# Optimization experiments

Measured on AMD Instinct MI355X. Metric: run time of the kernel, lower is better.

## Reference

```python
import jax, jax.numpy as jnp
import numpy as np
from jax import lax

B, D_MODEL, H, W = 8, 384, 64, 64
D_INNER, D_STATE, D_CONV, DT_RANK = 768, 16, 4, 24
C3, MLP_H = 3 * D_MODEL, 4 * D_MODEL
EPS = 1e-5


def setup_inputs():
    key = jax.random.key(0)
    ks = jax.random.split(key, 16)
    r = lambda i, shape, s=0.02: jax.random.normal(ks[i], shape, jnp.float32) * s
    return {
        'x': jax.random.normal(ks[0], (B, D_MODEL, H, W), jnp.float32),
        'ln1_g': jnp.ones((D_MODEL,), jnp.float32), 'ln1_b': jnp.zeros((D_MODEL,), jnp.float32),
        'in_w': r(1, (2 * D_INNER, D_MODEL)),
        'conv_w': r(2, (D_INNER, 1, D_CONV), 0.2), 'conv_b': jnp.zeros((D_INNER,), jnp.float32),
        'xproj_w': r(3, (DT_RANK + 2 * D_STATE, D_INNER)),
        'dtproj_w': r(4, (D_INNER, DT_RANK), 0.1),
        'dtproj_b': jnp.full((D_INNER,), jnp.log(jnp.expm1(0.01)).item(), jnp.float32),
        'A_log': jnp.log(jnp.broadcast_to(jnp.arange(1, D_STATE + 1, dtype=jnp.float32), (D_INNER, D_STATE))),
        'Dskip': jnp.ones((D_INNER,), jnp.float32),
        'out_w': r(5, (D_MODEL, D_INNER)),
        'dw_w': r(6, (C3, 1, 3, 3), 0.1),
        'bn_g': jnp.ones((C3,), jnp.float32), 'bn_b': jnp.zeros((C3,), jnp.float32),
        'bn_mean': jnp.zeros((C3,), jnp.float32), 'bn_var': jnp.ones((C3,), jnp.float32),
        'pw_w': r(7, (C3, C3)),
        'fus_w': r(8, (D_MODEL, D_MODEL)), 'fus_b': jnp.zeros((D_MODEL,), jnp.float32),
        'ln2_g': jnp.ones((D_MODEL,), jnp.float32), 'ln2_b': jnp.zeros((D_MODEL,), jnp.float32),
        'mlp_w1': r(9, (MLP_H, D_MODEL)), 'mlp_b1': jnp.zeros((MLP_H,), jnp.float32),
        'mlp_w2': r(10, (D_MODEL, MLP_H)), 'mlp_b2': jnp.zeros((D_MODEL,), jnp.float32),
    }


def _ln(x, g, b):
    m = x.mean(-1, keepdims=True)
    v = ((x - m) ** 2).mean(-1, keepdims=True)
    return (x - m) / jnp.sqrt(v + EPS) * g + b


def _dwt(x):
    x01 = x[:, :, 0::2, :] / 2
    x02 = x[:, :, 1::2, :] / 2
    x1, x3 = x01[:, :, :, 0::2], x01[:, :, :, 1::2]
    x2, x4 = x02[:, :, :, 0::2], x02[:, :, :, 1::2]
    ll = x1 + x2 + x3 + x4
    hl = -x1 - x2 + x3 + x4
    lh = -x1 + x2 - x3 + x4
    hh = x1 - x2 - x3 + x4
    return ll, jnp.concatenate([hl, lh, hh], axis=1)


def _idwt(ll, high):
    b, c, h, w = ll.shape
    hl, lh, hh = jnp.split(high, 3, axis=1)
    h_ll, h_hl, h_lh, h_hh = ll / 2, hl / 2, lh / 2, hh / 2
    y1 = h_ll - h_hl - h_lh + h_hh  # (even row, even col)
    y2 = h_ll - h_hl + h_lh - h_hh  # (odd row, even col)
    y3 = h_ll + h_hl - h_lh - h_hh  # (even row, odd col)
    y4 = h_ll + h_hl + h_lh + h_hh  # (odd row, odd col)
    row_e = jnp.stack([y1, y3], axis=-1).reshape(b, c, h, 2 * w)
    row_o = jnp.stack([y2, y4], axis=-1).reshape(b, c, h, 2 * w)
    return jnp.stack([row_e, row_o], axis=-2).reshape(b, c, 2 * h, 2 * w)


def _mamba(x, in_w, conv_w, conv_b, xproj_w, dtproj_w, dtproj_b, A_log, Dskip, out_w):
    # x: [B, L, d_model]
    bb = x.shape[0]
    xz = x @ in_w.T  # [B,L,2*d_inner]
    xi, z = jnp.split(xz, 2, axis=-1)
    xc = jnp.swapaxes(xi, 1, 2)  # [B,d_inner,L]
    xc = lax.conv_general_dilated(xc, conv_w, (1,), [(D_CONV - 1, 0)],
                                  feature_group_count=D_INNER,
                                  dimension_numbers=('NCH', 'OIH', 'NCH')) + conv_b[None, :, None]
    u = jax.nn.silu(jnp.swapaxes(xc, 1, 2))  # [B,L,d_inner]
    dbl = u @ xproj_w.T
    dtr = dbl[..., :DT_RANK]
    Bm = dbl[..., DT_RANK:DT_RANK + D_STATE]
    Cm = dbl[..., DT_RANK + D_STATE:]
    dt = jax.nn.softplus(dtr @ dtproj_w.T + dtproj_b)  # [B,L,d_inner]
    A = -jnp.exp(A_log)  # [d_inner,d_state]

    def step(h, t):
        dt_t, B_t, C_t, u_t = t
        dA = jnp.exp(dt_t[:, :, None] * A)
        h = dA * h + (dt_t * u_t)[:, :, None] * B_t[:, None, :]
        return h, jnp.sum(h * C_t[:, None, :], axis=-1)

    h0 = jnp.zeros((bb, D_INNER, D_STATE), x.dtype)
    xs = (jnp.swapaxes(dt, 0, 1), jnp.swapaxes(Bm, 0, 1), jnp.swapaxes(Cm, 0, 1), jnp.swapaxes(u, 0, 1))
    _, ys = lax.scan(step, h0, xs)
    y = jnp.swapaxes(ys, 0, 1) + u * Dskip
    y = y * jax.nn.silu(z)
    return y @ out_w.T


def reference(x, ln1_g, ln1_b, in_w, conv_w, conv_b, xproj_w, dtproj_w, dtproj_b,
              A_log, Dskip, out_w, dw_w, bn_g, bn_b, bn_mean, bn_var, pw_w,
              fus_w, fus_b, ln2_g, ln2_b, mlp_w1, mlp_b1, mlp_w2, mlp_b2):
    shortcut = x
    x_ll, x_high = _dwt(x)
    b, c, hh, ww = x_ll.shape
    # LL branch: LN -> Mamba -> residual
    x_ll_in = _ln(jnp.transpose(x_ll, (0, 2, 3, 1)), ln1_g, ln1_b)
    y = _mamba(x_ll_in.reshape(b, hh * ww, c), in_w, conv_w, conv_b, xproj_w,
               dtproj_w, dtproj_b, A_log, Dskip, out_w)
    x_ll_out = x_ll + jnp.transpose(y.reshape(b, hh, ww, c), (0, 3, 1, 2))
    # High-freq branch: depthwise3x3 -> BN(eval) -> SiLU -> 1x1 -> residual
    hd = lax.conv_general_dilated(x_high, dw_w, (1, 1), [(1, 1), (1, 1)],
                                  feature_group_count=C3,
                                  dimension_numbers=('NCHW', 'OIHW', 'NCHW'))
    hd = (hd - bn_mean[None, :, None, None]) / jnp.sqrt(bn_var + EPS)[None, :, None, None] \
         * bn_g[None, :, None, None] + bn_b[None, :, None, None]
    hd = jax.nn.silu(hd)
    x_high_out = x_high + jnp.einsum('bchw,oc->bohw', hd, pw_w)
    # Reconstruct + fusion 1x1 conv + residual
    recon = _idwt(x_ll_out, x_high_out)
    recon = jnp.einsum('bchw,oc->bohw', recon, fus_w) + fus_b[None, :, None, None]
    x2 = shortcut + recon
    # LN + MLP + residual
    xn = _ln(jnp.transpose(x2, (0, 2, 3, 1)), ln2_g, ln2_b)
    m = jax.nn.gelu(xn @ mlp_w1.T + mlp_b1, approximate=False) @ mlp_w2.T + mlp_b2
    return x2 + jnp.transpose(m, (0, 3, 1, 2))
```

## Files before the change

### kernel.cpp

```cpp
#include <hip/hip_runtime.h>
#include <hip/hip_bf16.h>
#include <math.h>

typedef __hip_bfloat16 bf16;
typedef __attribute__((ext_vector_type(8))) short bf16x8;
typedef __attribute__((ext_vector_type(4))) float f32x4;
typedef unsigned short u16;

#define LN_EPS 1e-5f

__device__ inline u16 f2b(float v) {
    __hip_bfloat16 h = __float2bfloat16(v);
    return *reinterpret_cast<u16*>(&h);
}

__device__ inline float b2f_lo(unsigned int w) { return __uint_as_float(w << 16); }
__device__ inline float b2f_hi(unsigned int w) { return __uint_as_float(w & 0xFFFF0000u); }

__device__ inline void gload_lds16(const void* g, void* l) {
    __builtin_amdgcn_global_load_lds(
        (const __attribute__((address_space(1))) void*)(uintptr_t)g,
        (__attribute__((address_space(3))) void*)(uintptr_t)(unsigned int)(uintptr_t)l,
        16, 0, 0);
}

__global__ __launch_bounds__(256) void sentinel_kernel(float* __restrict__ out, int n) {
    int i = blockIdx.x * 256 + threadIdx.x;
    if (i < n) out[i] = 123.0f;
}

__global__ __launch_bounds__(256) void reduce12_kernel(const float* __restrict__ P,
                                                       float* __restrict__ out, int n4) {
    int i = blockIdx.x * 256 + threadIdx.x;
    if (i >= n4) return;
    const float4* p4 = (const float4*)P;
    float4 s = p4[i];
#pragma unroll
    for (int z = 1; z < 12; z++) {
        float4 v = p4[(size_t)z * n4 + i];
        s.x += v.x; s.y += v.y; s.z += v.z; s.w += v.w;
    }
    ((float4*)out)[i] = s;
}

__global__ void detect_kernel(const unsigned int* __restrict__ g, int* __restrict__ flag) {
    *flag = (*g == 0x3F803F80u) ? 1 : 0;
}

struct Jobs {
    const void* src[25];
    int prefix[26];
};
__global__ __launch_bounds__(256) void convert_kernel(Jobs J, u16* __restrict__ dst16,
                                                      float* __restrict__ dst32,
                                                      const int* __restrict__ flag) {
    int i = blockIdx.x * 256 + threadIdx.x;
    int total = J.prefix[25];
    if (i >= total) return;
    int f = *flag;
    int lo = 0;
    while (J.prefix[lo + 1] <= i) lo++;
    int off = i - J.prefix[lo];
    float v = f ? (float)((const bf16*)J.src[lo])[off] : ((const float*)J.src[lo])[off];
    if (lo < 6) dst16[i] = f2b(v);
    else        dst32[i - J.prefix[6]] = v;
}

__global__ __launch_bounds__(256) void dwt_kernel(const void* __restrict__ xv,
                                                  float* __restrict__ xll,
                                                  float* __restrict__ xhigh,
                                                  const int* __restrict__ flag) {
    __shared__ float tile[32][133];
    int blk = blockIdx.x;
    int cc = blk % 12;
    int t2 = blk / 12;
    int i  = t2 % 32;
    int b  = t2 / 32;
    int t  = threadIdx.x;
    int c_l = t >> 3;
    int sub = t & 7;
    size_t rowbase = ((size_t)(b * 384 + cc * 32 + c_l)) * 4096 + (size_t)i * 128;
    if (*flag) {
        const u16* xp = (const u16*)xv + rowbase;
#pragma unroll
        for (int k = 0; k < 2; k++) {
            int e0 = (sub + k * 8) * 8;
            uint4 v = *(const uint4*)(xp + e0);
            tile[c_l][e0 + 0] = b2f_lo(v.x); tile[c_l][e0 + 1] = b2f_hi(v.x);
            tile[c_l][e0 + 2] = b2f_lo(v.y); tile[c_l][e0 + 3] = b2f_hi(v.y);
            tile[c_l][e0 + 4] = b2f_lo(v.z); tile[c_l][e0 + 5] = b2f_hi(v.z);
            tile[c_l][e0 + 6] = b2f_lo(v.w); tile[c_l][e0 + 7] = b2f_hi(v.w);
        }
    } else {
        const float* xp = (const float*)xv + rowbase;
#pragma unroll
        for (int k = 0; k < 4; k++) {
            int f0 = (sub + k * 8) * 4;
            float4 v = *(const float4*)(xp + f0);
            tile[c_l][f0 + 0] = v.x; tile[c_l][f0 + 1] = v.y;
            tile[c_l][f0 + 2] = v.z; tile[c_l][f0 + 3] = v.w;
        }
    }
    __syncthreads();
    int c_out = t & 31;
    int jg = t >> 5;
    int cg = cc * 32 + c_out;
#pragma unroll
    for (int jj = 0; jj < 4; jj++) {
        int j = jg * 4 + jj;
        float A = tile[c_out][2 * j];
        float B = tile[c_out][2 * j + 1];
        float C = tile[c_out][64 + 2 * j];
        float D = tile[c_out][64 + 2 * j + 1];
        float ll = 0.5f * (A + B + C + D);
        float hl = 0.5f * (B + D - A - C);
        float lh = 0.5f * (C + D - A - B);
        float hh = 0.5f * (A + D - B - C);
        int pm = b * 1024 + i * 32 + j;
        xll[(size_t)pm * 384 + cg] = ll;
        size_t hb = (size_t)pm * 1152;
        xhigh[hb + cg] = hl;
        xhigh[hb + 384 + cg] = lh;
        xhigh[hb + 768 + cg] = hh;
    }
}

template <bool OBF>
__global__ __launch_bounds__(128) void ln_kernel(const float* __restrict__ in,
                                                 void* __restrict__ outv,
                                                 const float* __restrict__ g,
                                                 const float* __restrict__ b) {
    const int C = 384;
    int row = blockIdx.x;
    int t = threadIdx.x;
    const float* rp = in + (size_t)row * C;
    float v0 = rp[t], v1 = rp[t + 128], v2 = rp[t + 256];
    __shared__ float red[128];
    red[t] = v0 + v1 + v2;
    __syncthreads();
    for (int off = 64; off > 0; off >>= 1) {
        if (t < off) red[t] += red[t + off];
        __syncthreads();
    }
    float mean = red[0] * (1.f / 384.f);
    __syncthreads();
    float d0 = v0 - mean, d1 = v1 - mean, d2 = v2 - mean;
    red[t] = d0 * d0 + d1 * d1 + d2 * d2;
    __syncthreads();
    for (int off = 64; off > 0; off >>= 1) {
        if (t < off) red[t] += red[t + off];
        __syncthreads();
    }
    float inv = rsqrtf(red[0] * (1.f / 384.f) + LN_EPS);
    float o0 = d0 * inv * g[t]       + b[t];
    float o1 = d1 * inv * g[t + 128] + b[t + 128];
    float o2 = d2 * inv * g[t + 256] + b[t + 256];
    if constexpr (OBF) {
        u16* op = (u16*)outv + (size_t)row * C;
        op[t] = f2b(o0); op[t + 128] = f2b(o1); op[t + 256] = f2b(o2);
    } else {
        float* op = (float*)outv + (size_t)row * C;
        op[t] = o0; op[t + 128] = o1; op[t + 256] = o2;
    }
}

#define EP_NONE 0
#define EP_SOFTPLUS_BIAS 1
#define EP_ADD 2
#define EP_FUS 3
#define EP_GELU_BIAS 4
#define EP_FINAL 5

template <int EPIL, bool CBF>
__global__ __launch_bounds__(256) void gemm_mfma(const u16* __restrict__ A, int lda,
                                                 const u16* __restrict__ W,
                                                 void* __restrict__ Cp, int ldc,
                                                 int M, int N, int K,
                                                 const float* __restrict__ addsrc,
                                                 const float* __restrict__ bias,
                                                 const void* __restrict__ xres,
                                                 void* __restrict__ obf,
                                                 int m_off,
                                                 const int* __restrict__ flag) {
    __shared__ u16 Als[128][32];
    __shared__ u16 Bls[128][32];
    const int t = threadIdx.x;
    const int wave = t >> 6, lane = t & 63;
    const int quad = lane >> 4, r16 = lane & 15;
    const int wm = (wave >> 1) * 64, wn = (wave & 1) * 64;
    const int mb = blockIdx.y * 128, nb = blockIdx.x * 128;
    f32x4 acc[4][4] = {};

    const int srow = wave * 32 + (lane >> 2);
    const int scol = (lane & 3) * 8;
    const u16* Ag0 = A + (size_t)(mb + srow) * lda + scol;
    const u16* Ag1 = A + (size_t)(mb + srow + 16) * lda + scol;
    const u16* Wg0 = W + (size_t)(nb + srow) * (size_t)K + scol;
    const u16* Wg1 = W + (size_t)(nb + srow + 16) * (size_t)K + scol;
    u16* Al0 = &Als[wave * 32][0];
    u16* Al1 = &Als[wave * 32 + 16][0];
    u16* Bl0 = &Bls[wave * 32][0];
    u16* Bl1 = &Bls[wave * 32 + 16][0];

    for (int k0 = 0; k0 < K; k0 += 32) {
        gload_lds16(Ag0 + k0, Al0);
        gload_lds16(Ag1 + k0, Al1);
        gload_lds16(Wg0 + k0, Bl0);
        gload_lds16(Wg1 + k0, Bl1);
        __syncthreads();
        bf16x8 af[4], bfv[4];
#pragma unroll
        for (int i = 0; i < 4; i++) af[i] = *(const bf16x8*)&Als[wm + i * 16 + r16][quad * 8];
#pragma unroll
        for (int j = 0; j < 4; j++) bfv[j] = *(const bf16x8*)&Bls[wn + j * 16 + r16][quad * 8];
#pragma unroll
        for (int i = 0; i < 4; i++)
#pragma unroll
            for (int j = 0; j < 4; j++)
                acc[i][j] = __builtin_amdgcn_mfma_f32_16x16x32_bf16(af[i], bfv[j], acc[i][j], 0, 0, 0);
        __syncthreads();
    }

    int f = 0;
    if constexpr (EPIL == EP_FUS || EPIL == EP_FINAL) f = *flag;
#pragma unroll
    for (int i = 0; i < 4; i++) {
#pragma unroll
        for (int j = 0; j < 4; j++) {
#pragma unroll
            for (int rg = 0; rg < 4; rg++) {
                int m = mb + wm + i * 16 + quad * 4 + rg;
                int n = nb + wn + j * 16 + r16;
                float v = acc[i][j][rg];
                if constexpr (EPIL == EP_NONE) {
                    if constexpr (CBF) ((u16*)Cp)[(size_t)m * ldc + n] = f2b(v);
                    else               ((float*)Cp)[(size_t)m * ldc + n] = v;
                } else if constexpr (EPIL == EP_ADD) {
                    ((float*)Cp)[(size_t)m * ldc + n] = addsrc[(size_t)m * ldc + n] + v;
                } else if constexpr (EPIL == EP_FUS) {
                    v += bias[n];
                    int bb = m >> 12, pix = m & 4095;
                    size_t xi = ((size_t)(bb * 384 + n) << 12) + pix;
                    v += f ? (float)((const bf16*)xres)[xi] : ((const float*)xres)[xi];
                    ((float*)Cp)[(size_t)m * ldc + n] = v;
                } else if constexpr (EPIL == EP_GELU_BIAS) {
                    v += bias[n];
                    v = 0.5f * v * (1.f + erff(v * 0.70710678118654752f));
                    if constexpr (CBF) ((u16*)Cp)[(size_t)m * ldc + n] = f2b(v);
                    else               ((float*)Cp)[(size_t)m * ldc + n] = v;
                } else if constexpr (EPIL == EP_FINAL) {
                    v += bias[n];
                    int gm = m_off + m;
                    v += addsrc[(size_t)gm * 384 + n];
                    int bb = gm >> 12, pix = gm & 4095;
                    size_t oi = ((size_t)(bb * 384 + n) << 12) + pix;
                    if (f) ((bf16*)obf)[oi] = __float2bfloat16(v);
                    else   ((float*)obf)[oi] = v;
                }
            }
        }
    }
}

template <int EPIL, bool SPLITK>
__global__ __launch_bounds__(256) void gemm_nt(const float* __restrict__ A, int lda,
                                               const float* __restrict__ W,
                                               float* __restrict__ C, int ldc,
                                               int M, int N, int K,
                                               const float* __restrict__ bias,
                                               int kc) {
    __shared__ __align__(16) float As[16][68];
    __shared__ __align__(16) float Bs[16][68];
    int t = threadIdx.x;
    int mb = blockIdx.y * 64;
    int nb = blockIdx.x * 64;
    int kb = SPLITK ? blockIdx.z * kc : 0;
    int ke = SPLITK ? kb + kc : K;
    int tm = t & 15, tn = t >> 4;
    float* Cout = C;
    if constexpr (SPLITK) Cout = C + (size_t)blockIdx.z * (size_t)M * ldc;
    float acc[4][4] = {};
    for (int k0 = kb; k0 < ke; k0 += 16) {
#pragma unroll
        for (int i = 0; i < 4; i++) {
            int idx = t + i * 256;
            int r = idx >> 4, c = idx & 15;
            float v = 0.f;
            if (k0 + c < K) v = A[(size_t)(mb + r) * lda + k0 + c];
            As[c][r] = v;
        }
#pragma unroll
        for (int i = 0; i < 4; i++) {
            int idx = t + i * 256;
            int r = idx >> 4, c = idx & 15;
            float v = 0.f;
            if ((nb + r) < N && (k0 + c) < K) v = W[(size_t)(nb + r) * K + k0 + c];
            Bs[c][r] = v;
        }
        __syncthreads();
#pragma unroll
        for (int kk = 0; kk < 16; kk++) {
            float4 av = *(const float4*)&As[kk][tm * 4];
            float4 bv = *(const float4*)&Bs[kk][tn * 4];
            float a4[4] = {av.x, av.y, av.z, av.w};
            float b4[4] = {bv.x, bv.y, bv.z, bv.w};
#pragma unroll
            for (int i = 0; i < 4; i++)
#pragma unroll
                for (int j = 0; j < 4; j++) acc[i][j] += a4[i] * b4[j];
        }
        __syncthreads();
    }
#pragma unroll
    for (int i = 0; i < 4; i++) {
        int m = mb + tm * 4 + i;
        if (m >= M) continue;
#pragma unroll
        for (int j = 0; j < 4; j++) {
            int n = nb + tn * 4 + j;
            if (n >= N) continue;
            float v = acc[i][j];
            if constexpr (SPLITK) {
                Cout[(size_t)m * ldc + n] = v;
            } else if constexpr (EPIL == EP_NONE) {
                C[(size_t)m * ldc + n] = v;
            } else if constexpr (EPIL == EP_SOFTPLUS_BIAS) {
                v += bias[n];
                v = (v > 20.f) ? v : log1pf(expf(v));
                C[(size_t)m * ldc + n] = v;
            }
        }
    }
}

__global__ __launch_bounds__(256) void conv1d_silu_kernel(const float* __restrict__ xz,
                                                          const float* __restrict__ cw,
                                                          const float* __restrict__ cb,
                                                          float* __restrict__ u) {
    int tid = blockIdx.x * 256 + threadIdx.x;
    int dq = tid % 192;
    int t2 = tid / 192;
    int l = t2 % 1024;
    int b = t2 / 1024;
    int d = dq * 4;
    float4 q0 = *(const float4*)&cw[d * 4];
    float4 q1 = *(const float4*)&cw[d * 4 + 4];
    float4 q2 = *(const float4*)&cw[d * 4 + 8];
    float4 q3 = *(const float4*)&cw[d * 4 + 12];
    float4 acc = *(const float4*)&cb[d];
    int rowbase = b * 1024;
#pragma unroll
    for (int k = 0; k < 4; k++) {
        int ls = l - 3 + k;
        if (ls < 0) continue;
        float4 xv = *(const float4*)&xz[(size_t)(rowbase + ls) * 1536 + d];
        acc.x += ((const float*)&q0)[k] * xv.x;
        acc.y += ((const float*)&q1)[k] * xv.y;
        acc.z += ((const float*)&q2)[k] * xv.z;
        acc.w += ((const float*)&q3)[k] * xv.w;
    }
    float4 o;
    o.x = acc.x / (1.f + __expf(-acc.x));
    o.y = acc.y / (1.f + __expf(-acc.y));
    o.z = acc.z / (1.f + __expf(-acc.z));
    o.w = acc.w / (1.f + __expf(-acc.w));
    *(float4*)&u[(size_t)(rowbase + l) * 768 + d] = o;
}

__device__ inline void scan_load_ac(const float* __restrict__ A_log, int d,
                                    float (&Ac)[16], bool& structured) {
#pragma unroll
    for (int s = 0; s < 16; s++) Ac[s] = -__expf(A_log[d * 16 + s]);
    structured = true;
#pragma unroll
    for (int s = 0; s < 16; s++)
        structured = structured && (fabsf(Ac[s] - (s + 1) * Ac[0]) <= 1e-5f * fabsf(Ac[s]));
}

__global__ __launch_bounds__(256) void scan_p1(const float* __restrict__ dt,
                                               const float* __restrict__ u,
                                               const float* __restrict__ dbl,
                                               const float* __restrict__ A_log,
                                               float* __restrict__ st) {
    int idx = blockIdx.x * 256 + threadIdx.x;
    int g = idx % 6144;
    int c = idx / 6144;
    int d = g % 768, b = g / 768;
    float Ac[16]; bool structured;
    scan_load_ac(A_log, d, Ac, structured);
    float h[16];
#pragma unroll
    for (int s = 0; s < 16; s++) h[s] = 0.f;
    float S = 0.f;
    size_t m0 = (size_t)b * 1024 + c * 128;
    if (structured) {
        for (int j = 0; j < 128; j++) {
            size_t m = m0 + j;
            float dtv = dt[m * 768 + d];
            float uv  = u[m * 768 + d];
            const float4* bp = (const float4*)(dbl + m * 56 + 24);
            float4 B0 = bp[0], B1 = bp[1], B2 = bp[2], B3 = bp[3];
            float Bv[16] = {B0.x,B0.y,B0.z,B0.w, B1.x,B1.y,B1.z,B1.w,
                            B2.x,B2.y,B2.z,B2.w, B3.x,B3.y,B3.z,B3.w};
            float du = dtv * uv;
            S += dtv;
            float q = __expf(dtv * Ac[0]);
            float a = q;
            h[0] = a * h[0] + du * Bv[0];
#pragma unroll
            for (int s = 1; s < 16; s++) { a *= q; h[s] = a * h[s] + du * Bv[s]; }
        }
    } else {
        for (int j = 0; j < 128; j++) {
            size_t m = m0 + j;
            float dtv = dt[m * 768 + d];
            float uv  = u[m * 768 + d];
            const float4* bp = (const float4*)(dbl + m * 56 + 24);
            float4 B0 = bp[0], B1 = bp[1], B2 = bp[2], B3 = bp[3];
            float Bv[16] = {B0.x,B0.y,B0.z,B0.w, B1.x,B1.y,B1.z,B1.w,
                            B2.x,B2.y,B2.z,B2.w, B3.x,B3.y,B3.z,B3.w};
            float du = dtv * uv;
            S += dtv;
#pragma unroll
            for (int s = 0; s < 16; s++) h[s] = __expf(dtv * Ac[s]) * h[s] + du * Bv[s];
        }
    }
    float* stp = st + (size_t)(c * 6144 + g) * 32;
#pragma unroll
    for (int s = 0; s < 16; s++) stp[s] = __expf(Ac[s] * S);
#pragma unroll
    for (int s = 0; s < 16; s++) stp[16 + s] = h[s];
}

__global__ __launch_bounds__(256) void scan_p2(float* __restrict__ st) {
    int tid = blockIdx.x * 256 + threadIdx.x;
    int s = tid & 15;
    int g = tid >> 4;
    float H = 0.f;
#pragma unroll
    for (int c = 0; c < 8; c++) {
        size_t i = (size_t)(c * 6144 + g) * 32;
        float P  = st[i + s];
        float hE = st[i + 16 + s];
        st[i + s] = H;
        H = hE + P * H;
    }
}

__global__ __launch_bounds__(256) void scan_p3(const float* __restrict__ dt,
                                               const float* __restrict__ u,
                                               const float* __restrict__ dbl,
                                               const float* __restrict__ z,
                                               const float* __restrict__ A_log,
                                               const float* __restrict__ Dskip,
                                               const float* __restrict__ st,
                                               u16* __restrict__ ybuf) {
    int idx = blockIdx.x * 256 + threadIdx.x;
    int g = idx % 6144;
    int c = idx / 6144;
    int d = g % 768, b = g / 768;
    float Ac[16]; bool structured;
    scan_load_ac(A_log, d, Ac, structured);
    float Dsk = Dskip[d];
    float h[16];
    const float* stp = st + (size_t)(c * 6144 + g) * 32;
#pragma unroll
    for (int s = 0; s < 16; s++) h[s] = stp[s];
    size_t m0 = (size_t)b * 1024 + c * 128;
    if (structured) {
        for (int j = 0; j < 128; j++) {
            size_t m = m0 + j;
            float dtv = dt[m * 768 + d];
            float uv  = u[m * 768 + d];
            float zv  = z[m * 1536 + 768 + d];
            const float4* bp = (const float4*)(dbl + m * 56 + 24);
            float4 B0 = bp[0], B1 = bp[1], B2 = bp[2], B3 = bp[3];
            float4 C0 = bp[4], C1 = bp[5], C2 = bp[6], C3 = bp[7];
            float Bv[16] = {B0.x,B0.y,B0.z,B0.w, B1.x,B1.y,B1.z,B1.w,
                            B2.x,B2.y,B2.z,B2.w, B3.x,B3.y,B3.z,B3.w};
            float Cv[16] = {C0.x,C0.y,C0.z,C0.w, C1.x,C1.y,C1.z,C1.w,
                            C2.x,C2.y,C2.z,C2.w, C3.x,C3.y,C3.z,C3.w};
            float du = dtv * uv;
            float q = __expf(dtv * Ac[0]);
            float a = q;
            h[0] = a * h[0] + du * Bv[0];
            float y = h[0] * Cv[0];
#pragma unroll
            for (int s = 1; s < 16; s++) {
                a *= q;
                h[s] = a * h[s] + du * Bv[s];
                y += h[s] * Cv[s];
            }
            float sig = 1.f / (1.f + __expf(-zv));
            ybuf[m * 3072 + d] = f2b((y + uv * Dsk) * (zv * sig));
        }
    } else {
        for (int j = 0; j < 128; j++) {
            size_t m = m0 + j;
            float dtv = dt[m * 768 + d];
            float uv  = u[m * 768 + d];
            float zv  = z[m * 1536 + 768 + d];
            const float4* bp = (const float4*)(dbl + m * 56 + 24);
            float4 B0 = bp[0], B1 = bp[1], B2 = bp[2], B3 = bp[3];
            float4 C0 = bp[4], C1 = bp[5], C2 = bp[6], C3 = bp[7];
            float Bv[16] = {B0.x,B0.y,B0.z,B0.w, B1.x,B1.y,B1.z,B1.w,
                            B2.x,B2.y,B2.z,B2.w, B3.x,B3.y,B3.z,B3.w};
            float Cv[16] = {C0.x,C0.y,C0.z,C0.w, C1.x,C1.y,C1.z,C1.w,
                            C2.x,C2.y,C2.z,C2.w, C3.x,C3.y,C3.z,C3.w};
            float du = dtv * uv;
            float y = 0.f;
#pragma unroll
            for (int s = 0; s < 16; s++) {
                h[s] = __expf(dtv * Ac[s]) * h[s] + du * Bv[s];
                y += h[s] * Cv[s];
            }
            float sig = 1.f / (1.f + __expf(-zv));
            ybuf[m * 3072 + d] = f2b((y + uv * Dsk) * (zv * sig));
        }
    }
}

__global__ __launch_bounds__(256) void dwconv_bn_silu_kernel(const float* __restrict__ xh,
                                                             const float* __restrict__ w,
                                                             const float* __restrict__ g,
                                                             const float* __restrict__ bb,
                                                             const float* __restrict__ mean,
                                                             const float* __restrict__ var,
                                                             u16* __restrict__ hd) {
    int tid = blockIdx.x * 256 + threadIdx.x;
    int cq = tid % 288;
    int t2 = tid / 288;
    int xc = t2 & 3;
    int t3 = t2 >> 2;
    int y = t3 % 32;
    int b = t3 / 32;
    int c = cq * 4;
    float wk[9][4];
#pragma unroll
    for (int i = 0; i < 4; i++) {
        float4 wa = *(const float4*)&w[(c + i) * 9];
        float4 wbv = *(const float4*)&w[(c + i) * 9 + 4];
        float wcv = w[(c + i) * 9 + 8];
        wk[0][i] = wa.x; wk[1][i] = wa.y; wk[2][i] = wa.z; wk[3][i] = wa.w;
        wk[4][i] = wbv.x; wk[5][i] = wbv.y; wk[6][i] = wbv.z; wk[7][i] = wbv.w;
        wk[8][i] = wcv;
    }
    float4 mn = *(const float4*)&mean[c];
    float4 vr = *(const float4*)&var[c];
    float4 gg = *(const float4*)&g[c];
    float4 bv = *(const float4*)&bb[c];
    float scl[4], sft[4];
    scl[0] = rsqrtf(vr.x + LN_EPS) * gg.x; sft[0] = bv.x - mn.x * scl[0];
    scl[1] = rsqrtf(vr.y + LN_EPS) * gg.y; sft[1] = bv.y - mn.y * scl[1];
    scl[2] = rsqrtf(vr.z + LN_EPS) * gg.z; sft[2] = bv.z - mn.z * scl[2];
    scl[3] = rsqrtf(vr.w + LN_EPS) * gg.w; sft[3] = bv.w - mn.w * scl[3];

    int x0 = xc * 8;
    size_t pixbase = (size_t)b * 1024 + y * 32;
    float win[3][3][4];
    auto ldcol = [&](int xx, float (&col)[3][4]) {
#pragma unroll
        for (int r = 0; r < 3; r++) {
            int yy = y + r - 1;
            if (xx < 0 || xx > 31 || yy < 0 || yy > 31) {
                col[r][0] = col[r][1] = col[r][2] = col[r][3] = 0.f;
            } else {
                float4 v = *(const float4*)&xh[((size_t)b * 1024 + yy * 32 + xx) * 1152 + c];
                col[r][0] = v.x; col[r][1] = v.y; col[r][2] = v.z; col[r][3] = v.w;
            }
        }
    };
    ldcol(x0 - 1, win[0]);
    ldcol(x0, win[1]);
#pragma unroll
    for (int xi = 0; xi < 8; xi++) {
        int x = x0 + xi;
        ldcol(x + 1, win[2]);
        ushort4 o;
        u16* op = (u16*)&o;
#pragma unroll
        for (int i = 0; i < 4; i++) {
            float acc = 0.f;
#pragma unroll
            for (int ky = 0; ky < 3; ky++)
#pragma unroll
                for (int kx = 0; kx < 3; kx++)
                    acc += wk[ky * 3 + kx][i] * win[kx][ky][i];
            float vv = acc * scl[i] + sft[i];
            op[i] = f2b(vv / (1.f + __expf(-vv)));
        }
        *(ushort4*)&hd[(pixbase + x) * 1152 + c] = o;
#pragma unroll
        for (int r = 0; r < 3; r++)
#pragma unroll
            for (int i = 0; i < 4; i++) {
                win[0][r][i] = win[1][r][i];
                win[1][r][i] = win[2][r][i];
            }
    }
}

__global__ __launch_bounds__(256) void idwt_kernel(const float* __restrict__ xll,
                                                   const float* __restrict__ xh,
                                                   u16* __restrict__ recon) {
    int idx = blockIdx.x * 256 + threadIdx.x;
    int c = idx % 384;
    int t = idx / 384;
    int p = t % 1024;
    int b = t / 1024;
    int i = p >> 5, j = p & 31;
    float ll = xll[(size_t)(b * 1024 + p) * 384 + c];
    int hb = (b * 1024 + p) * 1152;
    float hl = xh[hb + c];
    float lh = xh[hb + 384 + c];
    float hh = xh[hb + 768 + c];
    float y1 = 0.5f * (ll - hl - lh + hh);
    float y3 = 0.5f * (ll + hl - lh - hh);
    float y2 = 0.5f * (ll - hl + lh - hh);
    float y4 = 0.5f * (ll + hl + lh + hh);
    int r0 = b * 4096 + (2 * i) * 64 + 2 * j;
    recon[(size_t)r0 * 384 + c] = f2b(y1);
    recon[(size_t)(r0 + 1) * 384 + c] = f2b(y3);
    recon[(size_t)(r0 + 64) * 384 + c] = f2b(y2);
    recon[(size_t)(r0 + 65) * 384 + c] = f2b(y4);
}

extern "C" void kernel_launch(void* const* d_in, const int* in_sizes, int n_in,
                              void* d_out, int out_size, void* d_ws, size_t ws_size,
                              hipStream_t stream) {
    const void* x = d_in[0];
    void* out = d_out;

    float* ws = (float*)d_ws;
    float* x_ll    = ws;
    float* x_high  = ws + 3145728;
    u16*   mlp_hid = (u16*)ws;
    float* xz      = ws + 12582912;
    u16*   ybuf    = (u16*)xz;
    u16*   hd      = (u16*)xz;
    u16*   recon   = (u16*)(ws + 17301504);
    u16*   xn      = recon;
    float* u       = ws + 25165824;
    float* dt      = ws + 31457280;
    u16*   x_ll_in = (u16*)dt;
    float* xpart   = dt;
    float* x2      = ws + 25165824;
    float* dbl     = ws + 37748736;
    float* scanst  = ws + 38207488;

    u16* wb16 = (u16*)(ws + 39780352);
    u16* b_in_w   = wb16;
    u16* b_out_w  = wb16 + 589824;
    u16* b_pw_w   = wb16 + 884736;
    u16* b_fus_w  = wb16 + 2211840;
    u16* b_mlp_w1 = wb16 + 2359296;
    u16* b_mlp_w2 = wb16 + 2949120;
    float* f32base = ws + 39780352 + 1769472;
    float* c_conv_w   = f32base;
    float* c_conv_b   = f32base + 3072;
    float* c_xproj_w  = f32base + 3840;
    float* c_dtproj_w = f32base + 46848;
    float* c_dtproj_b = f32base + 65280;
    float* c_A_log    = f32base + 66048;
    float* c_Dskip    = f32base + 78336;
    float* c_dw_w     = f32base + 79104;
    float* c_bn_g     = f32base + 89472;
    float* c_bn_b     = f32base + 90624;
    float* c_bn_mean  = f32base + 91776;
    float* c_bn_var   = f32base + 92928;
    float* c_ln1_g    = f32base + 94080;
    float* c_ln1_b    = f32base + 94464;
    float* c_ln2_g    = f32base + 94848;
    float* c_ln2_b    = f32base + 95232;
    float* c_fus_b    = f32base + 95616;
    float* c_mlp_b1   = f32base + 96000;
    float* c_mlp_b2   = f32base + 97536;
    int* flag = (int*)(f32base + 97920);

    if (ws_size < (size_t)(39780352 + 1769472 + 97920 + 2) * 4) {
        sentinel_kernel<<<(out_size + 255) / 256, 256, 0, stream>>>((float*)out, out_size);
        return;
    }

    detect_kernel<<<1, 1, 0, stream>>>((const unsigned int*)d_in[1], flag);
    Jobs J;
    const int src_idx[25] = {3, 11, 17, 18, 22, 24,
                             4, 5, 6, 7, 8, 9, 10, 12, 13, 14, 15, 16,
                             1, 2, 20, 21, 19, 23, 25};
    const int joff[26] = {0, 589824, 884736, 2211840, 2359296, 2949120, 3538944,
                          3538944 + 3072, 3538944 + 3840, 3538944 + 46848, 3538944 + 65280,
                          3538944 + 66048, 3538944 + 78336, 3538944 + 79104, 3538944 + 89472,
                          3538944 + 90624, 3538944 + 91776, 3538944 + 92928, 3538944 + 94080,
                          3538944 + 94464, 3538944 + 94848, 3538944 + 95232, 3538944 + 95616,
                          3538944 + 96000, 3538944 + 97536, 3538944 + 97920};
    for (int i = 0; i < 25; i++) J.src[i] = d_in[src_idx[i]];
    for (int i = 0; i < 26; i++) J.prefix[i] = joff[i];
    convert_kernel<<<(3636864 + 255) / 256, 256, 0, stream>>>(J, wb16, f32base, flag);

    dwt_kernel<<<3072, 256, 0, stream>>>(x, x_ll, x_high, flag);
    ln_kernel<true><<<8192, 128, 0, stream>>>(x_ll, x_ll_in, c_ln1_g, c_ln1_b);
    gemm_mfma<EP_NONE, false><<<dim3(12, 64), 256, 0, stream>>>(x_ll_in, 384, b_in_w, xz, 1536,
                                                                8192, 1536, 384, nullptr, nullptr, nullptr, nullptr, 0, flag);
    conv1d_silu_kernel<<<6144, 256, 0, stream>>>(xz, c_conv_w, c_conv_b, u);
    gemm_nt<EP_NONE, true><<<dim3(1, 128, 12), 256, 0, stream>>>(u, 768, c_xproj_w, xpart, 56,
                                                                 8192, 56, 768, nullptr, 64);
    reduce12_kernel<<<(114688 + 255) / 256, 256, 0, stream>>>(xpart, dbl, 114688);
    gemm_nt<EP_SOFTPLUS_BIAS, false><<<dim3(12, 128), 256, 0, stream>>>(dbl, 56, c_dtproj_w, dt, 768,
                                                                        8192, 768, 24, c_dtproj_b, 0);
    scan_p1<<<192, 256, 0, stream>>>(dt, u, dbl, c_A_log, scanst);
    scan_p2<<<384, 256, 0, stream>>>(scanst);
    scan_p3<<<192, 256, 0, stream>>>(dt, u, dbl, xz, c_A_log, c_Dskip, scanst, ybuf);
    gemm_mfma<EP_ADD, false><<<dim3(3, 64), 256, 0, stream>>>(ybuf, 3072, b_out_w, x_ll, 384,
                                                              8192, 384, 768, x_ll, nullptr, nullptr, nullptr, 0, flag);
    dwconv_bn_silu_kernel<<<1152, 256, 0, stream>>>(x_high, c_dw_w, c_bn_g, c_bn_b, c_bn_mean, c_bn_var, hd);
    gemm_mfma<EP_ADD, false><<<dim3(9, 64), 256, 0, stream>>>(hd, 1152, b_pw_w, x_high, 1152,
                                                              8192, 1152, 1152, x_high, nullptr, nullptr, nullptr, 0, flag);
    idwt_kernel<<<12288, 256, 0, stream>>>(x_ll, x_high, recon);
    gemm_mfma<EP_FUS, false><<<dim3(3, 256), 256, 0, stream>>>(recon, 384, b_fus_w, x2, 384,
                                                               32768, 384, 384, nullptr, c_fus_b, x, nullptr, 0, flag);
    ln_kernel<true><<<32768, 128, 0, stream>>>(x2, xn, c_ln2_g, c_ln2_b);
    for (int ck = 0; ck < 2; ck++) {
        const u16* xn_c = xn + (size_t)ck * 16384 * 384;
        gemm_mfma<EP_GELU_BIAS, true><<<dim3(12, 128), 256, 0, stream>>>(xn_c, 384, b_mlp_w1, mlp_hid, 1536,
                                                                         16384, 1536, 384, nullptr, c_mlp_b1, nullptr, nullptr, 0, flag);
        gemm_mfma<EP_FINAL, false><<<dim3(3, 128), 256, 0, stream>>>(mlp_hid, 1536, b_mlp_w2, nullptr, 0,
                                                                     16384, 384, 1536, x2, c_mlp_b2, nullptr, out, ck * 16384, flag);
    }
}
```

Before: 810.2 us.

## Split selective scan into 16 chunks and store chunk states in xz scratch

The chunked Mamba scan now uses 16 chunks of 64 steps instead of 8 chunks of 128. This doubles the block count of the first and third scan passes from 192 to 384, so more compute units stay busy and each thread runs a shorter serial chain. The per-chunk state, which no longer fits the old scratch area, is written into the already-consumed x half of the xz buffer. The z half is left intact. The sequential loops also get unroll 2, and the cross-chunk combine pass now walks 16 chunks instead of 8.

```diff
diff --git a/kernel.cpp b/kernel.cpp
--- a/kernel.cpp
+++ b/kernel.cpp
@@ -22,6 +22,13 @@
         (const __attribute__((address_space(1))) void*)(uintptr_t)g,
         (__attribute__((address_space(3))) void*)(uintptr_t)(unsigned int)(uintptr_t)l,
         16, 0, 0);
+}
+
+__device__ inline float* st_ptr(float* base, int e) {
+    return base + (size_t)(e / 12) * 1536 + 384 + (e % 12) * 32;
+}
+__device__ inline const float* st_ptr(const float* base, int e) {
+    return base + (size_t)(e / 12) * 1536 + 384 + (e % 12) * 32;
 }
 
 __global__ __launch_bounds__(256) void sentinel_kernel(float* __restrict__ out, int n) {
@@ -381,7 +388,7 @@
                                                const float* __restrict__ u,
                                                const float* __restrict__ dbl,
                                                const float* __restrict__ A_log,
-                                               float* __restrict__ st) {
+                                               float* __restrict__ stbase) {
     int idx = blockIdx.x * 256 + threadIdx.x;
     int g = idx % 6144;
     int c = idx / 6144;
@@ -392,9 +399,10 @@
 #pragma unroll
     for (int s = 0; s < 16; s++) h[s] = 0.f;
     float S = 0.f;
-    size_t m0 = (size_t)b * 1024 + c * 128;
+    size_t m0 = (size_t)b * 1024 + c * 64;
     if (structured) {
-        for (int j = 0; j < 128; j++) {
+#pragma unroll 2
+        for (int j = 0; j < 64; j++) {
             size_t m = m0 + j;
             float dtv = dt[m * 768 + d];
             float uv  = u[m * 768 + d];
@@ -411,7 +419,8 @@
             for (int s = 1; s < 16; s++) { a *= q; h[s] = a * h[s] + du * Bv[s]; }
         }
     } else {
-        for (int j = 0; j < 128; j++) {
+#pragma unroll 2
+        for (int j = 0; j < 64; j++) {
             size_t m = m0 + j;
             float dtv = dt[m * 768 + d];
             float uv  = u[m * 768 + d];
@@ -425,24 +434,24 @@
             for (int s = 0; s < 16; s++) h[s] = __expf(dtv * Ac[s]) * h[s] + du * Bv[s];
         }
     }
-    float* stp = st + (size_t)(c * 6144 + g) * 32;
+    float* stp = st_ptr(stbase, c * 6144 + g);
 #pragma unroll
     for (int s = 0; s < 16; s++) stp[s] = __expf(Ac[s] * S);
 #pragma unroll
     for (int s = 0; s < 16; s++) stp[16 + s] = h[s];
 }
 
-__global__ __launch_bounds__(256) void scan_p2(float* __restrict__ st) {
+__global__ __launch_bounds__(256) void scan_p2(float* __restrict__ stbase) {
     int tid = blockIdx.x * 256 + threadIdx.x;
     int s = tid & 15;
     int g = tid >> 4;
     float H = 0.f;
 #pragma unroll
-    for (int c = 0; c < 8; c++) {
-        size_t i = (size_t)(c * 6144 + g) * 32;
-        float P  = st[i + s];
-        float hE = st[i + 16 + s];
-        st[i + s] = H;
+    for (int c = 0; c < 16; c++) {
+        float* p = st_ptr(stbase, c * 6144 + g);
+        float P  = p[s];
+        float hE = p[16 + s];
+        p[s] = H;
         H = hE + P * H;
     }
 }
@@ -453,7 +462,7 @@
                                                const float* __restrict__ z,
                                                const float* __restrict__ A_log,
                                                const float* __restrict__ Dskip,
-                                               const float* __restrict__ st,
+                                               const float* __restrict__ stbase,
                                                u16* __restrict__ ybuf) {
     int idx = blockIdx.x * 256 + threadIdx.x;
     int g = idx % 6144;
@@ -463,12 +472,13 @@
     scan_load_ac(A_log, d, Ac, structured);
     float Dsk = Dskip[d];
     float h[16];
-    const float* stp = st + (size_t)(c * 6144 + g) * 32;
+    const float* stp = st_ptr(stbase, c * 6144 + g);
 #pragma unroll
     for (int s = 0; s < 16; s++) h[s] = stp[s];
-    size_t m0 = (size_t)b * 1024 + c * 128;
+    size_t m0 = (size_t)b * 1024 + c * 64;
     if (structured) {
-        for (int j = 0; j < 128; j++) {
+#pragma unroll 2
+        for (int j = 0; j < 64; j++) {
             size_t m = m0 + j;
             float dtv = dt[m * 768 + d];
             float uv  = u[m * 768 + d];
@@ -495,7 +505,8 @@
             ybuf[m * 3072 + d] = f2b((y + uv * Dsk) * (zv * sig));
         }
     } else {
-        for (int j = 0; j < 128; j++) {
+#pragma unroll 2
+        for (int j = 0; j < 64; j++) {
             size_t m = m0 + j;
             float dtv = dt[m * 768 + d];
             float uv  = u[m * 768 + d];
@@ -646,7 +657,6 @@
     float* xpart   = dt;
     float* x2      = ws + 25165824;
     float* dbl     = ws + 37748736;
-    float* scanst  = ws + 38207488;
 
     u16* wb16 = (u16*)(ws + 39780352);
     u16* b_in_w   = wb16;
@@ -707,9 +717,9 @@
     reduce12_kernel<<<(114688 + 255) / 256, 256, 0, stream>>>(xpart, dbl, 114688);
     gemm_nt<EP_SOFTPLUS_BIAS, false><<<dim3(12, 128), 256, 0, stream>>>(dbl, 56, c_dtproj_w, dt, 768,
                                                                         8192, 768, 24, c_dtproj_b, 0);
-    scan_p1<<<192, 256, 0, stream>>>(dt, u, dbl, c_A_log, scanst);
-    scan_p2<<<384, 256, 0, stream>>>(scanst);
-    scan_p3<<<192, 256, 0, stream>>>(dt, u, dbl, xz, c_A_log, c_Dskip, scanst, ybuf);
+    scan_p1<<<384, 256, 0, stream>>>(dt, u, dbl, c_A_log, xz);
+    scan_p2<<<384, 256, 0, stream>>>(xz);
+    scan_p3<<<384, 256, 0, stream>>>(dt, u, dbl, xz, c_A_log, c_Dskip, xz, ybuf);
     gemm_mfma<EP_ADD, false><<<dim3(3, 64), 256, 0, stream>>>(ybuf, 3072, b_out_w, x_ll, 384,
                                                               8192, 384, 768, x_ll, nullptr, nullptr, nullptr, 0, flag);
     dwconv_bn_silu_kernel<<<1152, 256, 0, stream>>>(x_high, c_dw_w, c_bn_g, c_bn_b, c_bn_mean, c_bn_var, hd);
```

After: 831.2 us. 2.6% more time.
